# Performance work log

Hardware: AMD Instinct MI355X
Metric: run time of the kernel (lower is better)

The kernel has to match this reference:

```python
import jax, jax.numpy as jnp
import numpy as np

KERNEL = 3
PAD = (KERNEL - 1) // 2  # non-causal symmetric padding


def setup_inputs() -> dict:
    key = jax.random.key(0)
    k1, k2, k3 = jax.random.split(key, 3)
    B, Cin, Cout, S = 16, 64, 64, 1024
    return {
        "input": jax.random.normal(k1, (B, Cin, S), dtype=jnp.float32),
        "weight": jax.random.normal(k2, (Cout, Cin, S, KERNEL), dtype=jnp.float32),
        "bias": jax.random.normal(k3, (Cout, S), dtype=jnp.float32),
    }


def reference(input, weight, bias):
    # input: (B, Cin, S); weight: (Cout, Cin, S, K); bias: (Cout, S)
    S = input.shape[-1]
    padded = jnp.pad(input, ((0, 0), (0, 0), (PAD, PAD)))
    # unfolded windows: (B, Cin, S, K) -- small, avoids the (B,Cout,Cin,S,K) blowup
    unfolded = jnp.stack([padded[:, :, k:k + S] for k in range(KERNEL)], axis=-1)
    # position-specific (non-weight-shared) conv: contract Cin and K per position s
    out = jnp.einsum("bcsk,ocsk->bos", unfolded, weight)
    return out + bias[None, :, :]
```

## Files before the change

kernel.cpp:

```cpp
#include <hip/hip_runtime.h>

namespace {
constexpr int CIN = 64, COUT = 64, SS = 1024, KK = 3;
constexpr int STL = 4;
constexpr int POS = STL + 2;
constexpr int NCG = 8, CPG = 8;
}

__global__ __launch_bounds__(512, 2)
void locon1d(const float* __restrict__ in, const float* __restrict__ wt,
             const float* __restrict__ bias, float* __restrict__ out) {
  __shared__ float smem[8192];

  const int tid = threadIdx.x;
  const int sl  = tid & 3;
  const int og  = (tid >> 2) & 15;
  const int cg  = tid >> 6;
  const int bid = blockIdx.x;
  const int st  = ((bid & 7) << 5) + (bid >> 3);
  const int s0  = st * STL;
  const int s   = s0 + sl;
  const int o0  = og * 4;
  const int cb  = cg * CPG;

  #pragma unroll
  for (int i = 0; i < 3; ++i) {
    const int t  = tid + i * 512;
    const int c  = t / 24;
    const int r  = t - c * 24;
    const int bq = r / 6;
    const int p  = r - bq * 6;
    const int sg = s0 - 1 + p;
    const bool v = (unsigned)sg < (unsigned)SS;
    const float* ip = in + ((size_t)(4 * bq) * CIN + c) * SS + sg;
    float4 x4;
    x4.x = v ? ip[0] : 0.f;
    x4.y = v ? ip[(size_t)1 * CIN * SS] : 0.f;
    x4.z = v ? ip[(size_t)2 * CIN * SS] : 0.f;
    x4.w = v ? ip[(size_t)3 * CIN * SS] : 0.f;
    *reinterpret_cast<float4*>(&smem[(c * POS + p) * 16 + 4 * bq]) = x4;
  }
  __syncthreads();

  float w[CPG][4][KK];
  #pragma unroll
  for (int oo = 0; oo < 4; ++oo) {
    const float* wp = wt + (((size_t)(o0 + oo) * CIN + cb) * SS + s) * KK;
    #pragma unroll
    for (int c = 0; c < CPG; ++c)
      #pragma unroll
      for (int k = 0; k < KK; ++k)
        w[c][oo][k] = wp[(size_t)c * SS * KK + k];
  }

  float acc[4][16];
  #pragma unroll
  for (int oo = 0; oo < 4; ++oo)
    #pragma unroll
    for (int b = 0; b < 16; ++b) acc[oo][b] = 0.f;

  #pragma unroll
  for (int c = 0; c < CPG; ++c) {
    #pragma unroll
    for (int k = 0; k < KK; ++k) {
      const float* base = &smem[((cb + c) * POS + sl + k) * 16];
      #pragma unroll
      for (int g = 0; g < 4; ++g) {
        const float4 x4 = *reinterpret_cast<const float4*>(base + 4 * g);
        #pragma unroll
        for (int oo = 0; oo < 4; ++oo) {
          const float wv = w[c][oo][k];
          acc[oo][4 * g + 0] += wv * x4.x;
          acc[oo][4 * g + 1] += wv * x4.y;
          acc[oo][4 * g + 2] += wv * x4.z;
          acc[oo][4 * g + 3] += wv * x4.w;
        }
      }
    }
  }

  #pragma unroll
  for (int oo = 0; oo < 4; ++oo) {
    __syncthreads();
    #pragma unroll
    for (int b = 0; b < 16; ++b)
      smem[cg * 1024 + (b * 16 + og) * 4 + sl] = acc[oo][b];
    __syncthreads();
    #pragma unroll
    for (int i = 0; i < 2; ++i) {
      const int item = tid + i * 512;
      float sum = 0.f;
      #pragma unroll
      for (int g = 0; g < NCG; ++g) sum += smem[g * 1024 + item];
      const int b   = item >> 6;
      const int rem = item & 63;
      const int o   = (rem >> 2) * 4 + oo;
      const int s2  = s0 + (rem & 3);
      out[((size_t)b * COUT + o) * SS + s2] = sum + bias[o * SS + s2];
    }
  }
}

extern "C" void kernel_launch(void* const* d_in, const int* in_sizes, int n_in,
                              void* d_out, int out_size, void* d_ws, size_t ws_size,
                              hipStream_t stream) {
  const float* in = (const float*)d_in[0];
  const float* wt = (const float*)d_in[1];
  const float* bs = (const float*)d_in[2];
  float* out = (float*)d_out;
  hipLaunchKernelGGL(locon1d, dim3(256), dim3(512), 0, stream, in, wt, bs, out);
}
```

Measured before the change: 100.5 us.

## Stage weight loads through per-wave LDS transpose with coalesced float4 prefetch

Replaces the per-thread scalar weight gathers with float4 loads laid out contiguously across each wave. The loaded values are transposed through a double-buffered per-wave LDS slab and then read back as float4 per output channel. The next channel's weights are prefetched into registers while the current channel's FMAs run. This targets poor coalescing on the dominant weight stream. It raises LDS use to roughly 104KB per block, which likely limits residency to one block per CU. It also depends on wave-lockstep ordering rather than a barrier for the LDS hand-off.

```diff
diff --git a/kernel.cpp b/kernel.cpp
--- a/kernel.cpp
+++ b/kernel.cpp
@@ -5,21 +5,25 @@
 constexpr int STL = 4;
 constexpr int POS = STL + 2;
 constexpr int NCG = 8, CPG = 8;
+constexpr int WROW  = 20;
+constexpr int WSLAB = COUT * WROW;
+constexpr int WOFF  = CIN * POS * 16;
+constexpr int SMEMDW = WOFF + NCG * 2 * WSLAB;
 }
 
 __global__ __launch_bounds__(512, 2)
 void locon1d(const float* __restrict__ in, const float* __restrict__ wt,
              const float* __restrict__ bias, float* __restrict__ out) {
-  __shared__ float smem[8192];
+  __shared__ float smem[SMEMDW];
 
-  const int tid = threadIdx.x;
-  const int sl  = tid & 3;
-  const int og  = (tid >> 2) & 15;
-  const int cg  = tid >> 6;
-  const int bid = blockIdx.x;
+  const int tid  = threadIdx.x;
+  const int sl   = tid & 3;
+  const int og   = (tid >> 2) & 15;
+  const int cg   = tid >> 6;
+  const int lane = tid & 63;
+  const int bid  = blockIdx.x;
   const int st  = ((bid & 7) << 5) + (bid >> 3);
   const int s0  = st * STL;
-  const int s   = s0 + sl;
   const int o0  = og * 4;
   const int cb  = cg * CPG;
 
@@ -42,16 +46,22 @@
   }
   __syncthreads();
 
-  float w[CPG][4][KK];
+  int wg[3];
+  int wd[3][4];
   #pragma unroll
-  for (int oo = 0; oo < 4; ++oo) {
-    const float* wp = wt + (((size_t)(o0 + oo) * CIN + cb) * SS + s) * KK;
+  for (int r = 0; r < 3; ++r) {
+    const int idx = r * 64 + lane;
+    const int oR  = idx / 3;
+    const int pR  = idx - oR * 3;
+    wg[r] = oR * (CIN * SS * KK) + pR * 4 + s0 * KK;
     #pragma unroll
-    for (int c = 0; c < CPG; ++c)
-      #pragma unroll
-      for (int k = 0; k < KK; ++k)
-        w[c][oo][k] = wp[(size_t)c * SS * KK + k];
+    for (int j = 0; j < 4; ++j) {
+      const int f  = pR * 4 + j;
+      const int fs = f / 3;
+      wd[r][j] = oR * WROW + fs * 4 + (f - fs * 3);
+    }
   }
+  float* const wlds = &smem[WOFF + cg * (2 * WSLAB)];
 
   float acc[4][16];
   #pragma unroll
@@ -59,25 +69,57 @@
     #pragma unroll
     for (int b = 0; b < 16; ++b) acc[oo][b] = 0.f;
 
-  #pragma unroll
-  for (int c = 0; c < CPG; ++c) {
-    #pragma unroll
-    for (int k = 0; k < KK; ++k) {
-      const float* base = &smem[((cb + c) * POS + sl + k) * 16];
-      #pragma unroll
-      for (int g = 0; g < 4; ++g) {
-        const float4 x4 = *reinterpret_cast<const float4*>(base + 4 * g);
-        #pragma unroll
-        for (int oo = 0; oo < 4; ++oo) {
-          const float wv = w[c][oo][k];
-          acc[oo][4 * g + 0] += wv * x4.x;
-          acc[oo][4 * g + 1] += wv * x4.y;
-          acc[oo][4 * g + 2] += wv * x4.z;
-          acc[oo][4 * g + 3] += wv * x4.w;
-        }
-      }
-    }
-  }
+  float4 wA[3], wB[3];
+
+  #define WLOAD(DST, C_) do {                                                  \
+    _Pragma("unroll")                                                          \
+    for (int r = 0; r < 3; ++r)                                                \
+      DST[r] = *reinterpret_cast<const float4*>(wt + wg[r] + (C_) * (SS * KK));\
+  } while (0)
+
+  WLOAD(wA, cb + 0);
+  WLOAD(wB, cb + 1);
+
+  #define WSTEP(WREG, CC) do {                                                 \
+    float* const wb = wlds + ((CC) & 1) * WSLAB;                               \
+    _Pragma("unroll")                                                          \
+    for (int r = 0; r < 3; ++r) {                                              \
+      wb[wd[r][0]] = WREG[r].x;                                                \
+      wb[wd[r][1]] = WREG[r].y;                                                \
+      wb[wd[r][2]] = WREG[r].z;                                                \
+      wb[wd[r][3]] = WREG[r].w;                                                \
+    }                                                                          \
+    if ((CC) + 2 < CPG) WLOAD(WREG, cb + (CC) + 2);                            \
+    float4 wq[4];                                                              \
+    _Pragma("unroll")                                                          \
+    for (int oo = 0; oo < 4; ++oo)                                             \
+      wq[oo] = *reinterpret_cast<const float4*>(&wb[(o0 + oo) * WROW + sl * 4]);\
+    const int c_ = cb + (CC);                                                  \
+    _Pragma("unroll")                                                          \
+    for (int k = 0; k < KK; ++k) {                                             \
+      const float* base_ = &smem[(c_ * POS + sl + k) * 16];                    \
+      _Pragma("unroll")                                                        \
+      for (int g = 0; g < 4; ++g) {                                            \
+        const float4 x4 = *reinterpret_cast<const float4*>(base_ + 4 * g);     \
+        _Pragma("unroll")                                                      \
+        for (int oo = 0; oo < 4; ++oo) {                                       \
+          const float wv = (k == 0) ? wq[oo].x : (k == 1) ? wq[oo].y : wq[oo].z;\
+          acc[oo][4 * g + 0] += wv * x4.x;                                     \
+          acc[oo][4 * g + 1] += wv * x4.y;                                     \
+          acc[oo][4 * g + 2] += wv * x4.z;                                     \
+          acc[oo][4 * g + 3] += wv * x4.w;                                     \
+        }                                                                      \
+      }                                                                        \
+    }                                                                          \
+  } while (0)
+
+  WSTEP(wA, 0); WSTEP(wB, 1);
+  WSTEP(wA, 2); WSTEP(wB, 3);
+  WSTEP(wA, 4); WSTEP(wB, 5);
+  WSTEP(wA, 6); WSTEP(wB, 7);
+
+  #undef WSTEP
+  #undef WLOAD
 
   #pragma unroll
   for (int oo = 0; oo < 4; ++oo) {
```

Result: slower. 160.9 us (+60.1%).
